# Optimization experiments

Measured on AMD Instinct MI355X. Metric: run time of the kernel, lower is better.

## Reference

```python
import jax, jax.numpy as jnp
import numpy as np

B = 16384      # number of graphs
NODES = 11     # nodes per graph (fixed by h.view(N/11, 11, F))
N = B * NODES  # total nodes
IN = 256       # in_dim
H = 256        # hidden_dim
DEG = 8        # avg degree
E = N * DEG    # total edges
NC = 2         # n_classes


def setup_inputs() -> dict:
    key = jax.random.key(0)
    ks = jax.random.split(key, 24)
    feature = jax.random.normal(ks[0], (N, IN), jnp.float32)
    # intra-graph random edges: local ids in [0,11), offset per graph
    src_l = jax.random.randint(ks[1], (B, NODES * DEG), 0, NODES)
    dst_l = jax.random.randint(ks[2], (B, NODES * DEG), 0, NODES)
    off = (jnp.arange(B, dtype=jnp.int32) * NODES)[:, None]
    src = (src_l + off).reshape(-1).astype(jnp.int32)
    dst = (dst_l + off).reshape(-1).astype(jnp.int32)

    def w(k, shape, fan_in):
        return jax.random.normal(k, shape, jnp.float32) * (1.0 / np.sqrt(fan_in))

    return {
        'feature': feature, 'src': src, 'dst': dst,
        'W1': w(ks[3], (IN, H), IN), 'b1': jnp.zeros((H,), jnp.float32),
        'W2': w(ks[4], (H, H), H),  'b2': jnp.zeros((H,), jnp.float32),
        'W3': w(ks[5], (H, 8), H),  'b3': jnp.zeros((8,), jnp.float32),
        'Wih': w(ks[6], (4 * H, IN), IN), 'Whh': w(ks[7], (4 * H, H), H),
        'bih': jnp.zeros((4 * H,), jnp.float32), 'bhh': jnp.zeros((4 * H,), jnp.float32),
        'Wf1': w(ks[8], (H, 64), H), 'bf1': jnp.zeros((64,), jnp.float32),
        'Wf2': w(ks[9], (64, 2), 64), 'bf2': jnp.zeros((2,), jnp.float32),
        'Wc': w(ks[10], (8, NC), 8), 'bc': jnp.zeros((NC,), jnp.float32),
    }


def _deg_norms(src, dst):
    ones = jnp.ones(src.shape[0], jnp.float32)
    out_deg = jnp.clip(jax.ops.segment_sum(ones, src, num_segments=N), 1.0)
    in_deg = jnp.clip(jax.ops.segment_sum(ones, dst, num_segments=N), 1.0)
    return out_deg ** -0.5, in_deg ** -0.5  # DGL GraphConv norm='both'


def _gconv(feat, W, b, src, dst, sn, dn):
    x = (feat * sn[:, None]) @ W                     # src-normalize then project
    agg = jax.ops.segment_sum(x[src], dst, num_segments=N)  # SpMM message passing
    return agg * dn[:, None] + b


def _lstm_last(x, Wih, Whh, bih, bhh):
    # x: [B, T, IN]; PyTorch gate order i,f,g,o; returns last hidden [B, H]
    h0 = jnp.zeros((x.shape[0], H), x.dtype)
    c0 = jnp.zeros((x.shape[0], H), x.dtype)
    bias = bih + bhh

    def step(carry, xt):
        h, c = carry
        gates = xt @ Wih.T + h @ Whh.T + bias
        i, f, g, o = jnp.split(gates, 4, axis=-1)
        c = jax.nn.sigmoid(f) * c + jax.nn.sigmoid(i) * jnp.tanh(g)
        h = jax.nn.sigmoid(o) * jnp.tanh(c)
        return (h, c), None

    (h, _), _ = jax.lax.scan(step, (h0, c0), jnp.swapaxes(x, 0, 1))
    return h


def reference(feature, src, dst, W1, b1, W2, b2, W3, b3,
              Wih, Whh, bih, bhh, Wf1, bf1, Wf2, bf2, Wc, bc):
    # LSTM branch over per-graph sequences of 11 node feature vectors
    hgru = feature.reshape(B, NODES, IN)
    h_last = _lstm_last(hgru, Wih, Whh, bih, bhh)
    out = (h_last @ Wf1 + bf1) @ Wf2 + bf2           # ff (dropout = identity, eval)

    # GraphConv branch
    sn, dn = _deg_norms(src, dst)
    h = jax.nn.relu(_gconv(feature, W1, b1, src, dst, sn, dn))
    h = jnp.tanh(_gconv(h, W2, b2, src, dst, sn, dn))
    h = jax.nn.relu(_gconv(h, W3, b3, src, dst, sn, dn))

    hg = h.reshape(B, NODES, 8).mean(axis=1)          # dgl.mean_nodes
    y = hg @ Wc + bc                                  # classify1 (dropout = identity)
    return y + out
```

## Files before the change

### kernel.cpp

```cpp
#include <hip/hip_runtime.h>
#include <hip/hip_bf16.h>
#include <type_traits>

using u16 = unsigned short;

static constexpr int BG   = 16384;
static constexpr int NPG  = 11;
static constexpr int NTOT = BG * NPG;
static constexpr int EDG  = NTOT * 8;

typedef __attribute__((ext_vector_type(8))) short short8;
typedef __attribute__((ext_vector_type(4))) float f32x4;

__device__ __forceinline__ u16 f2bf(float f) {
  unsigned u = __float_as_uint(f);
  return (u16)((u + 0x7FFFu + ((u >> 16) & 1u)) >> 16);
}
__device__ __forceinline__ float bf2f(u16 u) { return __uint_as_float(((unsigned)u) << 16); }
__device__ __forceinline__ unsigned pk(float a, float b) {
  return (unsigned)f2bf(a) | ((unsigned)f2bf(b) << 16);
}
__device__ __forceinline__ float fast_sig(float x) {
  return __builtin_amdgcn_rcpf(1.f + __expf(-x));
}
__device__ __forceinline__ float fast_tanh(float x) {
  float a = fabsf(x);
  float e = __expf(-2.f * a);
  float t = (1.f - e) * __builtin_amdgcn_rcpf(1.f + e);
  return copysignf(t, x);
}

__global__ __launch_bounds__(1024, 4) void lstm_all(const float* __restrict__ feat,
                                                    u16* __restrict__ h,
                                                    const u16* __restrict__ Wp,
                                                    const float* __restrict__ biasP) {
  __shared__ u16 Ax[64 * 256];
  __shared__ u16 Ah[2][64 * 256];
  const int tid  = threadIdx.x;
  const int lane = tid & 63;
  const int wave = tid >> 6;
  const int q = lane >> 4;
  const int l = lane & 15;
  const int row0 = blockIdx.x * 64;

  #pragma unroll
  for (int p = 0; p < 2; ++p)
    *(uint4*)&Ah[0][(p * 1024 + tid) * 8] = uint4{0, 0, 0, 0};

  float creg[2][2][4];
  #pragma unroll
  for (int p = 0; p < 2; ++p)
    #pragma unroll
    for (int i = 0; i < 2; ++i)
      #pragma unroll
      for (int j = 0; j < 4; ++j) creg[p][i][j] = 0.f;

  float4 bias4[2][2];
  #pragma unroll
  for (int p = 0; p < 2; ++p)
    #pragma unroll
    for (int i = 0; i < 2; ++i)
      bias4[p][i] = *(const float4*)&biasP[(wave * 16 + p * 8 + i * 4 + q) * 4];

  const u16* wpA = Wp + (size_t)(wave * 64 + l) * 512 + q * 8;

  for (int t = 0; t < NPG; ++t) {
    const u16* AhR = Ah[t & 1];
    u16*       AhW = Ah[(t + 1) & 1];

    #pragma unroll
    for (int p = 0; p < 2; ++p) {
      const int idx = p * 1024 + tid;
      const int sr = idx >> 5;
      const int cc = idx & 31;
      const int kk = cc >> 2, s2 = cc & 3;
      const float* fp = feat + (size_t)(row0 + sr) * 2816 + t * 256 + cc * 8;
      float4 f0 = *(const float4*)fp;
      float4 f1 = *(const float4*)(fp + 4);
      uint4 v;
      v.x = pk(f0.x, f0.y); v.y = pk(f0.z, f0.w);
      v.z = pk(f1.x, f1.y); v.w = pk(f1.z, f1.w);
      *(uint4*)&Ax[kk * 2048 + (((sr << 2) + (s2 ^ (sr & 3)))) * 8] = v;
    }
    __syncthreads();

    #pragma unroll
    for (int p = 0; p < 2; ++p) {
      f32x4 acc[2][4] = {};
      #pragma unroll 4
      for (int kk = 0; kk < 8; ++kk) {
        const u16* Bsrc = &Ax[kk * 2048];
        short8 wf[2];
        #pragma unroll
        for (int i = 0; i < 2; ++i)
          wf[i] = *(const short8*)(wpA + (size_t)(p * 32 + i * 16) * 512 + kk * 32);
        #pragma unroll
        for (int j = 0; j < 4; ++j) {
          const int b = j * 16 + l;
          short8 xf = *(const short8*)&Bsrc[(((b << 2) + (q ^ (b & 3)))) * 8];
          #pragma unroll
          for (int i = 0; i < 2; ++i)
            acc[i][j] = __builtin_amdgcn_mfma_f32_16x16x32_bf16(wf[i], xf, acc[i][j], 0, 0, 0);
        }
      }
      #pragma unroll 4
      for (int kk = 0; kk < 8; ++kk) {
        const u16* Bsrc = &AhR[kk * 2048];
        short8 wf[2];
        #pragma unroll
        for (int i = 0; i < 2; ++i)
          wf[i] = *(const short8*)(wpA + (size_t)(p * 32 + i * 16) * 512 + (kk + 8) * 32);
        #pragma unroll
        for (int j = 0; j < 4; ++j) {
          const int b = j * 16 + l;
          short8 xf = *(const short8*)&Bsrc[(((b << 2) + (q ^ (b & 3)))) * 8];
          #pragma unroll
          for (int i = 0; i < 2; ++i)
            acc[i][j] = __builtin_amdgcn_mfma_f32_16x16x32_bf16(wf[i], xf, acc[i][j], 0, 0, 0);
        }
      }
      #pragma unroll
      for (int i = 0; i < 2; ++i) {
        const int u = wave * 16 + p * 8 + i * 4 + q;
        const float4 bb = bias4[p][i];
        const int kk2 = u >> 5, c2 = (u >> 3) & 3, e = u & 7;
        #pragma unroll
        for (int j = 0; j < 4; ++j) {
          const float gi = acc[i][j][0] + bb.x;
          const float gf = acc[i][j][1] + bb.y;
          const float gg = acc[i][j][2] + bb.z;
          const float go = acc[i][j][3] + bb.w;
          const float cn = fast_sig(gf) * creg[p][i][j] + fast_sig(gi) * fast_tanh(gg);
          creg[p][i][j] = cn;
          const float hv = fast_sig(go) * fast_tanh(cn);
          const u16 hb = f2bf(hv);
          const int b = j * 16 + l;
          AhW[kk2 * 2048 + (((b << 2) + (c2 ^ (b & 3)))) * 8 + e] = hb;
          if (t == NPG - 1) h[(size_t)(row0 + b) * 256 + u] = hb;
        }
      }
    }
    __syncthreads();
  }
}

template<int AMODE, typename TC>
__global__ __launch_bounds__(512) void gemm_mfma(const float* __restrict__ Af,
                                                 const u16* Ab,
                                                 const u16* __restrict__ Bt,
                                                 TC* C, int N, int K) {
  __shared__ u16 Alds[128 * 32];
  __shared__ u16 Blds[256 * 32];
  const int tid  = threadIdx.x;
  const int lane = tid & 63;
  const int wave = tid >> 6;
  const int q = lane >> 4;
  const int l = lane & 15;
  const int wm = (wave >> 2) * 64;
  const int wn = (wave & 3) * 64;
  const int row0 = blockIdx.y * 128;
  const int col0 = blockIdx.x * 256;

  f32x4 acc[4][4] = {};
  const int sr = tid >> 2;
  const int sq = tid & 3;
  const int aslot = sq ^ (sr & 3);

  for (int k0 = 0; k0 < K; k0 += 32) {
    {
      uint4 v;
      if constexpr (AMODE == 0) {
        const float* p = Af + (size_t)(row0 + sr) * K + k0 + sq * 8;
        float4 f0 = *(const float4*)p;
        float4 f1 = *(const float4*)(p + 4);
        v.x = pk(f0.x, f0.y); v.y = pk(f0.z, f0.w);
        v.z = pk(f1.x, f1.y); v.w = pk(f1.z, f1.w);
      } else {
        v = *(const uint4*)(Ab + (size_t)(row0 + sr) * K + k0 + sq * 8);
      }
      *(uint4*)&Alds[(((sr << 2) + aslot)) << 3] = v;
    }
    #pragma unroll
    for (int i = 0; i < 2; ++i) {
      const int n = sr + i * 128;
      const int slot = sq ^ (n & 3);
      uint4 v = *(const uint4*)(Bt + (size_t)(col0 + n) * K + k0 + sq * 8);
      *(uint4*)&Blds[(((n << 2) + slot)) << 3] = v;
    }
    __syncthreads();
    short8 af[4], bfr[4];
    #pragma unroll
    for (int i = 0; i < 4; ++i) {
      const int r = wm + i * 16 + l;
      af[i] = *(const short8*)&Alds[(((r << 2) + (q ^ (r & 3)))) << 3];
    }
    #pragma unroll
    for (int j = 0; j < 4; ++j) {
      const int n = wn + j * 16 + l;
      bfr[j] = *(const short8*)&Blds[(((n << 2) + (q ^ (n & 3)))) << 3];
    }
    #pragma unroll
    for (int i = 0; i < 4; ++i)
      #pragma unroll
      for (int j = 0; j < 4; ++j)
        acc[i][j] = __builtin_amdgcn_mfma_f32_16x16x32_bf16(af[i], bfr[j], acc[i][j], 0, 0, 0);
    __syncthreads();
  }
  #pragma unroll
  for (int i = 0; i < 4; ++i) {
    #pragma unroll
    for (int j = 0; j < 4; ++j) {
      #pragma unroll
      for (int r = 0; r < 4; ++r) {
        const int row = row0 + wm + i * 16 + q * 4 + r;
        const int col = col0 + wn + j * 16 + l;
        if constexpr (std::is_same<TC, float>::value)
          C[(size_t)row * N + col] = acc[i][j][r];
        else
          C[(size_t)row * N + col] = f2bf(acc[i][j][r]);
      }
    }
  }
}

__global__ __launch_bounds__(256) void k_prep_lstm_w(const float* __restrict__ Wih,
                                                     const float* __restrict__ Whh,
                                                     const float* __restrict__ bih,
                                                     const float* __restrict__ bhh,
                                                     u16* __restrict__ Wp,
                                                     float* __restrict__ biasP) {
  const int idx = blockIdx.x * 256 + threadIdx.x;
  const int np = idx >> 9, k = idx & 511;
  const int u = np >> 2, g = np & 3;
  const int n = g * 256 + u;
  const float v = (k < 256) ? Wih[n * 256 + k] : Whh[n * 256 + (k - 256)];
  Wp[idx] = f2bf(v);
  if (k == 0) biasP[np] = bih[n] + bhh[n];
}

__global__ __launch_bounds__(256) void k_transpose_w(const float* __restrict__ W,
                                                     u16* __restrict__ Wt) {
  const int idx = blockIdx.x * 256 + threadIdx.x;
  const int n = idx >> 8, k = idx & 255;
  Wt[idx] = f2bf(W[k * 256 + n]);
}

__global__ __launch_bounds__(256) void ff_kernel(const u16* __restrict__ h,
                                                 const float* __restrict__ Wf1,
                                                 const float* __restrict__ bf1,
                                                 const float* __restrict__ Wf2,
                                                 const float* __restrict__ bf2,
                                                 float* __restrict__ ffout) {
  __shared__ float hrow[16][256];
  __shared__ float tmp[16][64];
  const int tid = threadIdx.x;
  const int b0 = blockIdx.x * 16;
  for (int i = tid; i < 16 * 256; i += 256)
    hrow[i >> 8][i & 255] = bf2f(h[(size_t)(b0 + (i >> 8)) * 256 + (i & 255)]);
  __syncthreads();
  const int n = tid & 63, r = tid >> 6;
  float a0 = bf1[n], a1 = a0, a2 = a0, a3 = a0;
  #pragma unroll 8
  for (int k = 0; k < 256; ++k) {
    const float w = Wf1[k * 64 + n];
    a0 += hrow[r][k] * w;
    a1 += hrow[r + 4][k] * w;
    a2 += hrow[r + 8][k] * w;
    a3 += hrow[r + 12][k] * w;
  }
  tmp[r][n] = a0; tmp[r + 4][n] = a1; tmp[r + 8][n] = a2; tmp[r + 12][n] = a3;
  __syncthreads();
  if (tid < 32) {
    const int rr = tid >> 1, jj = tid & 1;
    float o = bf2[jj];
    #pragma unroll
    for (int k2 = 0; k2 < 64; ++k2) o += tmp[rr][k2] * Wf2[k2 * 2 + jj];
    ffout[(size_t)(b0 + rr) * 2 + jj] = o;
  }
}

__global__ __launch_bounds__(256) void k_graph_mats(const int* __restrict__ src,
                                                    const int* __restrict__ dst,
                                                    float* __restrict__ Mg) {
  constexpr int GPB = 32;
  __shared__ float Ms[GPB * 121];
  __shared__ float od[GPB * NPG];
  __shared__ float idg[GPB * NPG];
  const int tid = threadIdx.x;
  const int g0 = blockIdx.x * GPB;
  for (int i = tid; i < GPB * 121; i += 256) Ms[i] = 0.f;
  for (int i = tid; i < GPB * NPG; i += 256) { od[i] = 0.f; idg[i] = 0.f; }
  __syncthreads();
  const int ebase = g0 * 88;
  int ls[11], ld[11];
  #pragma unroll
  for (int i = 0; i < 11; ++i) {
    const int e = ebase + tid + i * 256;
    const int s = src[e], d = dst[e];
    const int g = s / NPG;
    const int gl = g - g0;
    ls[i] = gl * NPG + (s - g * NPG);
    ld[i] = gl * NPG + (d - g * NPG);
    atomicAdd(&od[ls[i]], 1.f);
    atomicAdd(&idg[ld[i]], 1.f);
  }
  __syncthreads();
  for (int i = tid; i < GPB * NPG; i += 256) {
    od[i]  = rsqrtf(fmaxf(od[i], 1.f));
    idg[i] = rsqrtf(fmaxf(idg[i], 1.f));
  }
  __syncthreads();
  #pragma unroll
  for (int i = 0; i < 11; ++i) {
    const int gl  = ls[i] / NPG;
    const int lsl = ls[i] - gl * NPG;
    const int ldl = ld[i] - gl * NPG;
    atomicAdd(&Ms[gl * 121 + ldl * NPG + lsl], od[ls[i]] * idg[ld[i]]);
  }
  __syncthreads();
  for (int i = tid; i < GPB * 121; i += 256) Mg[(size_t)g0 * 121 + i] = Ms[i];
}

template<int ACT>
__global__ __launch_bounds__(256) void k_mapply(const u16* __restrict__ Y,
                                                const float* __restrict__ Mg,
                                                const float* __restrict__ bias,
                                                u16* __restrict__ X) {
  __shared__ float Ms[121];
  const int g = blockIdx.x, c = threadIdx.x;
  if (c < 121) Ms[c] = Mg[(size_t)g * 121 + c];
  float y[NPG];
  const u16* yp = Y + (size_t)g * NPG * 256 + c;
  #pragma unroll
  for (int s = 0; s < NPG; ++s) y[s] = bf2f(yp[s * 256]);
  const float bc_ = bias[c];
  __syncthreads();
  u16* xp = X + (size_t)g * NPG * 256 + c;
  #pragma unroll
  for (int d = 0; d < NPG; ++d) {
    float z = bc_;
    #pragma unroll
    for (int s = 0; s < NPG; ++s) z += Ms[d * NPG + s] * y[s];
    if (ACT == 0) z = fmaxf(z, 0.f); else z = fast_tanh(z);
    xp[d * 256] = f2bf(z);
  }
}

__global__ __launch_bounds__(256) void k_gemm3(const u16* __restrict__ X,
                                               const float* __restrict__ W3,
                                               float* __restrict__ Y3) {
  __shared__ float W3s[2048];
  const int tid = threadIdx.x;
  for (int i = tid; i < 2048; i += 256) W3s[i] = W3[i];
  __syncthreads();
  const int r = tid >> 3, j = tid & 7;
  const int row = blockIdx.x * 32 + r;
  const u16* xp = X + (size_t)row * 256;
  float acc = 0.f;
  #pragma unroll 4
  for (int k = 0; k < 256; ++k) acc += bf2f(xp[k]) * W3s[k * 8 + j];
  Y3[(size_t)row * 8 + j] = acc;
}

__global__ __launch_bounds__(256) void k_final(const float* __restrict__ Y3,
                                               const float* __restrict__ Mg,
                                               const float* __restrict__ b3,
                                               const float* __restrict__ Wc,
                                               const float* __restrict__ bc,
                                               const float* __restrict__ ffout,
                                               float* __restrict__ out) {
  __shared__ float Ms[32][121];
  __shared__ float hg[32][8];
  const int tid = threadIdx.x;
  const int g0 = blockIdx.x * 32;
  for (int i = tid; i < 32 * 121; i += 256) Ms[i / 121][i % 121] = Mg[(size_t)g0 * 121 + i];
  const int gl = tid >> 3, j = tid & 7;
  const int g = g0 + gl;
  float y[NPG];
  #pragma unroll
  for (int s = 0; s < NPG; ++s) y[s] = Y3[((size_t)g * NPG + s) * 8 + j];
  __syncthreads();
  const float bj = b3[j];
  float accm = 0.f;
  #pragma unroll
  for (int d = 0; d < NPG; ++d) {
    float z = bj;
    #pragma unroll
    for (int s = 0; s < NPG; ++s) z += Ms[gl][d * NPG + s] * y[s];
    accm += fmaxf(z, 0.f);
  }
  hg[gl][j] = accm * (1.0f / 11.0f);
  __syncthreads();
  if (j < 2) {
    float o = bc[j];
    #pragma unroll
    for (int qq = 0; qq < 8; ++qq) o += hg[gl][qq] * Wc[qq * 2 + j];
    out[(size_t)g * 2 + j] = o + ffout[(size_t)g * 2 + j];
  }
}

extern "C" void kernel_launch(void* const* d_in, const int* in_sizes, int n_in,
                              void* d_out, int out_size, void* d_ws, size_t ws_size,
                              hipStream_t stream) {
  (void)in_sizes; (void)n_in; (void)out_size; (void)ws_size;
  const float* feature = (const float*)d_in[0];
  const int*   src     = (const int*)d_in[1];
  const int*   dst     = (const int*)d_in[2];
  const float* W1  = (const float*)d_in[3];
  const float* b1  = (const float*)d_in[4];
  const float* W2  = (const float*)d_in[5];
  const float* b2  = (const float*)d_in[6];
  const float* W3  = (const float*)d_in[7];
  const float* b3  = (const float*)d_in[8];
  const float* Wih = (const float*)d_in[9];
  const float* Whh = (const float*)d_in[10];
  const float* bih = (const float*)d_in[11];
  const float* bhh = (const float*)d_in[12];
  const float* Wf1 = (const float*)d_in[13];
  const float* bf1 = (const float*)d_in[14];
  const float* Wf2 = (const float*)d_in[15];
  const float* bf2 = (const float*)d_in[16];
  const float* Wc  = (const float*)d_in[17];
  const float* bc  = (const float*)d_in[18];
  float* out = (float*)d_out;

  char* ws = (char*)d_ws;
  float* ffout = (float*)ws;
  u16*   Wp    = (u16*)(ws + 131072);
  u16*   Wt1   = (u16*)(ws + 1179648);
  u16*   Wt2   = (u16*)(ws + 1310720);
  float* biasP = (float*)(ws + 1441792);
  float* Mg    = (float*)(ws + 1445888);
  u16*   Abuf  = (u16*)(ws + 9375744);
  u16*   hbuf  = (u16*)(ws + 9375744);
  float* Y3    = (float*)(ws + 101650432);

  k_prep_lstm_w<<<2048, 256, 0, stream>>>(Wih, Whh, bih, bhh, Wp, biasP);
  k_transpose_w<<<256, 256, 0, stream>>>(W1, Wt1);
  k_transpose_w<<<256, 256, 0, stream>>>(W2, Wt2);

  lstm_all<<<BG / 64, 1024, 0, stream>>>(feature, hbuf, Wp, biasP);
  ff_kernel<<<BG / 16, 256, 0, stream>>>(hbuf, Wf1, bf1, Wf2, bf2, ffout);

  k_graph_mats<<<BG / 32, 256, 0, stream>>>(src, dst, Mg);

  gemm_mfma<0, u16><<<dim3(1, NTOT / 128), 512, 0, stream>>>(feature, nullptr, Wt1, Abuf, 256, 256);
  k_mapply<0><<<BG, 256, 0, stream>>>(Abuf, Mg, b1, Abuf);

  gemm_mfma<1, u16><<<dim3(1, NTOT / 128), 512, 0, stream>>>(nullptr, Abuf, Wt2, Abuf, 256, 256);
  k_mapply<1><<<BG, 256, 0, stream>>>(Abuf, Mg, b2, Abuf);

  k_gemm3<<<NTOT / 32, 256, 0, stream>>>(Abuf, W3, Y3);
  k_final<<<BG / 32, 256, 0, stream>>>(Y3, Mg, b3, Wc, bc, ffout, out);
}
```

Measured before the change: 882.0 us.

## Pre-swizzle LSTM weights into MFMA fragment order and pad LDS chunks

The LSTM weight prep kernel now writes weights in per-wave, per-lane MFMA fragment order, so each lane's weight load in the recurrent loop becomes a contiguous coalesced 16-byte read instead of a strided one. The LDS tiles for x and h get a padded chunk stride (2056) and a new XOR swizzle to cut bank conflicts on fragment reads and scattered h writes. Bias moves into LDS instead of being held in registers, which may ease register pressure but adds LDS reads and raises shared-memory use per block.

Result: faster. 727.6 us (-17.5%).

```diff
diff --git a/kernel.cpp b/kernel.cpp
--- a/kernel.cpp
+++ b/kernel.cpp
@@ -32,10 +32,12 @@
 
 __global__ __launch_bounds__(1024, 4) void lstm_all(const float* __restrict__ feat,
                                                     u16* __restrict__ h,
-                                                    const u16* __restrict__ Wp,
+                                                    const u16* __restrict__ WfP,
                                                     const float* __restrict__ biasP) {
-  __shared__ u16 Ax[64 * 256];
-  __shared__ u16 Ah[2][64 * 256];
+  constexpr int CHUNK = 2056;
+  __shared__ u16 Ax[8 * CHUNK];
+  __shared__ u16 Ah[2][8 * CHUNK];
+  __shared__ float bLds[1024];
   const int tid  = threadIdx.x;
   const int lane = tid & 63;
   const int wave = tid >> 6;
@@ -43,9 +45,8 @@
   const int l = lane & 15;
   const int row0 = blockIdx.x * 64;
 
-  #pragma unroll
-  for (int p = 0; p < 2; ++p)
-    *(uint4*)&Ah[0][(p * 1024 + tid) * 8] = uint4{0, 0, 0, 0};
+  bLds[tid] = biasP[tid];
+  for (int i = tid; i < 8 * CHUNK / 2; i += 1024) ((unsigned*)Ah[0])[i] = 0u;
 
   float creg[2][2][4];
   #pragma unroll
@@ -55,14 +56,7 @@
       #pragma unroll
       for (int j = 0; j < 4; ++j) creg[p][i][j] = 0.f;
 
-  float4 bias4[2][2];
-  #pragma unroll
-  for (int p = 0; p < 2; ++p)
-    #pragma unroll
-    for (int i = 0; i < 2; ++i)
-      bias4[p][i] = *(const float4*)&biasP[(wave * 16 + p * 8 + i * 4 + q) * 4];
-
-  const u16* wpA = Wp + (size_t)(wave * 64 + l) * 512 + q * 8;
+  const u16* wfBase = WfP + ((size_t)wave << 15) + (lane << 3);
 
   for (int t = 0; t < NPG; ++t) {
     const u16* AhR = Ah[t & 1];
@@ -80,7 +74,7 @@
       uint4 v;
       v.x = pk(f0.x, f0.y); v.y = pk(f0.z, f0.w);
       v.z = pk(f1.x, f1.y); v.w = pk(f1.z, f1.w);
-      *(uint4*)&Ax[kk * 2048 + (((sr << 2) + (s2 ^ (sr & 3)))) * 8] = v;
+      *(uint4*)&Ax[kk * CHUNK + (((sr << 2) + (s2 ^ ((sr >> 1) & 3)))) * 8] = v;
     }
     __syncthreads();
 
@@ -89,15 +83,15 @@
       f32x4 acc[2][4] = {};
       #pragma unroll 4
       for (int kk = 0; kk < 8; ++kk) {
-        const u16* Bsrc = &Ax[kk * 2048];
+        const u16* Bsrc = &Ax[kk * CHUNK];
         short8 wf[2];
         #pragma unroll
         for (int i = 0; i < 2; ++i)
-          wf[i] = *(const short8*)(wpA + (size_t)(p * 32 + i * 16) * 512 + kk * 32);
+          wf[i] = *(const short8*)(wfBase + kk * 2048 + (p * 2 + i) * 512);
         #pragma unroll
         for (int j = 0; j < 4; ++j) {
           const int b = j * 16 + l;
-          short8 xf = *(const short8*)&Bsrc[(((b << 2) + (q ^ (b & 3)))) * 8];
+          short8 xf = *(const short8*)&Bsrc[(((b << 2) + (q ^ ((b >> 1) & 3)))) * 8];
           #pragma unroll
           for (int i = 0; i < 2; ++i)
             acc[i][j] = __builtin_amdgcn_mfma_f32_16x16x32_bf16(wf[i], xf, acc[i][j], 0, 0, 0);
@@ -105,15 +99,15 @@
       }
       #pragma unroll 4
       for (int kk = 0; kk < 8; ++kk) {
-        const u16* Bsrc = &AhR[kk * 2048];
+        const u16* Bsrc = &AhR[kk * CHUNK];
         short8 wf[2];
         #pragma unroll
         for (int i = 0; i < 2; ++i)
-          wf[i] = *(const short8*)(wpA + (size_t)(p * 32 + i * 16) * 512 + (kk + 8) * 32);
+          wf[i] = *(const short8*)(wfBase + (kk + 8) * 2048 + (p * 2 + i) * 512);
         #pragma unroll
         for (int j = 0; j < 4; ++j) {
           const int b = j * 16 + l;
-          short8 xf = *(const short8*)&Bsrc[(((b << 2) + (q ^ (b & 3)))) * 8];
+          short8 xf = *(const short8*)&Bsrc[(((b << 2) + (q ^ ((b >> 1) & 3)))) * 8];
           #pragma unroll
           for (int i = 0; i < 2; ++i)
             acc[i][j] = __builtin_amdgcn_mfma_f32_16x16x32_bf16(wf[i], xf, acc[i][j], 0, 0, 0);
@@ -121,8 +115,8 @@
       }
       #pragma unroll
       for (int i = 0; i < 2; ++i) {
-        const int u = wave * 16 + p * 8 + i * 4 + q;
-        const float4 bb = bias4[p][i];
+        const int u = wave * 16 + (p * 2 + i) * 4 + q;
+        const float4 bb = *(const float4*)&bLds[u * 4];
         const int kk2 = u >> 5, c2 = (u >> 3) & 3, e = u & 7;
         #pragma unroll
         for (int j = 0; j < 4; ++j) {
@@ -135,7 +129,7 @@
           const float hv = fast_sig(go) * fast_tanh(cn);
           const u16 hb = f2bf(hv);
           const int b = j * 16 + l;
-          AhW[kk2 * 2048 + (((b << 2) + (c2 ^ (b & 3)))) * 8 + e] = hb;
+          AhW[kk2 * CHUNK + (((b << 2) + (c2 ^ ((b >> 1) & 3)))) * 8 + e] = hb;
           if (t == NPG - 1) h[(size_t)(row0 + b) * 256 + u] = hb;
         }
       }
@@ -227,14 +221,22 @@
                                                      const float* __restrict__ Whh,
                                                      const float* __restrict__ bih,
                                                      const float* __restrict__ bhh,
-                                                     u16* __restrict__ Wp,
+                                                     u16* __restrict__ WfP,
                                                      float* __restrict__ biasP) {
   const int idx = blockIdx.x * 256 + threadIdx.x;
-  const int np = idx >> 9, k = idx & 511;
+  const int e = idx & 7;
+  const int lane = (idx >> 3) & 63;
+  const int chunk = idx >> 9;
+  const int f = chunk & 3;
+  const int kk = (chunk >> 2) & 15;
+  const int w = chunk >> 6;
+  const int q = lane >> 4, l = lane & 15;
+  const int np = w * 64 + f * 16 + l;
+  const int k = kk * 32 + q * 8 + e;
   const int u = np >> 2, g = np & 3;
   const int n = g * 256 + u;
   const float v = (k < 256) ? Wih[n * 256 + k] : Whh[n * 256 + (k - 256)];
-  Wp[idx] = f2bf(v);
+  WfP[idx] = f2bf(v);
   if (k == 0) biasP[np] = bih[n] + bhh[n];
 }
 
@@ -426,7 +428,7 @@
 
   char* ws = (char*)d_ws;
   float* ffout = (float*)ws;
-  u16*   Wp    = (u16*)(ws + 131072);
+  u16*   WfP   = (u16*)(ws + 131072);
   u16*   Wt1   = (u16*)(ws + 1179648);
   u16*   Wt2   = (u16*)(ws + 1310720);
   float* biasP = (float*)(ws + 1441792);
@@ -435,11 +437,11 @@
   u16*   hbuf  = (u16*)(ws + 9375744);
   float* Y3    = (float*)(ws + 101650432);
 
-  k_prep_lstm_w<<<2048, 256, 0, stream>>>(Wih, Whh, bih, bhh, Wp, biasP);
+  k_prep_lstm_w<<<2048, 256, 0, stream>>>(Wih, Whh, bih, bhh, WfP, biasP);
   k_transpose_w<<<256, 256, 0, stream>>>(W1, Wt1);
   k_transpose_w<<<256, 256, 0, stream>>>(W2, Wt2);
 
-  lstm_all<<<BG / 64, 1024, 0, stream>>>(feature, hbuf, Wp, biasP);
+  lstm_all<<<BG / 64, 1024, 0, stream>>>(feature, hbuf, WfP, biasP);
   ff_kernel<<<BG / 16, 256, 0, stream>>>(hbuf, Wf1, bf1, Wf2, bf2, ffout);
 
   k_graph_mats<<<BG / 32, 256, 0, stream>>>(src, dst, Mg);
```
